# Performance work log

Hardware: AMD Instinct MI355X
Metric: run time of the kernel (lower is better)

The kernel has to match this reference:

```python
import jax, jax.numpy as jnp
import numpy as np

B = 8
C = 256
NS = [16384, 4096, 1024, 256, 1]  # point-pyramid sizes per level
D = 3                              # coordinate dim
EPS = (1e-06, 1e-06, 1e-06, 1e-06, 1e-06)


def _pm_level(x, coords_c, coords_n, idx, p_i, eps_i):
    """One hierarchical gather-weighted power-mean pooling step.
    x: (B, C, N)  coords_c: (B, N, D)  coords_n: (B, Nn, D)  idx: (B, N) in [0, Nn).
    Returns pooled features (B, C, Nn)."""
    Bq, Cq, N = x.shape
    Nn = coords_n.shape[1]
    Dd = coords_c.shape[-1]
    # gather parent coords for each child, delta to parent
    cn = jnp.take_along_axis(coords_n, idx[:, :, None], axis=1)            # (B,N,D)
    delta = coords_c - cn                                                   # (B,N,D)
    # per-parent max/min of delta (scatter_max / scatter_min)
    smax = jax.vmap(lambda d, ix: jax.ops.segment_max(d, ix, num_segments=Nn))(delta, idx)
    smin = jax.vmap(lambda d, ix: jax.ops.segment_min(d, ix, num_segments=Nn))(delta, idx)
    pos_ub = jnp.maximum(smax, 0.0)   # clamp(min=0)
    neg_lb = jnp.minimum(smin, 0.0)   # clamp(max=0)
    # gather bounds back to children, pick by sign of delta
    pos_g = jnp.take_along_axis(pos_ub, idx[:, :, None], axis=1)
    neg_g = jnp.take_along_axis(neg_lb, idx[:, :, None], axis=1)
    inuse = jnp.where(delta >= 0.0, pos_g, neg_g)
    w = 1.0 - jnp.abs(delta) / (jnp.abs(inuse) + 1e-6)                      # (B,N,D)
    # split channels across the D coordinate weights: [q, q, ..., q+r]
    q, r = Cq // Dd, Cq % Dd
    reps = np.asarray([q] * (Dd - 1) + [q + r])
    w_c = jnp.repeat(w, reps, axis=-1, total_repeat_length=Cq)              # (B,N,C)
    x_pow = jnp.maximum(x, eps_i) ** p_i                                    # (B,C,N)
    xw = x_pow.transpose(0, 2, 1) * w_c                                     # (B,N,C)
    # scatter_sum of weighted powers and of weights, per parent cell
    xw_s = jax.vmap(lambda a, ix: jax.ops.segment_sum(a, ix, num_segments=Nn))(xw, idx)   # (B,Nn,C)
    w_s = jax.vmap(lambda a, ix: jax.ops.segment_sum(a, ix, num_segments=Nn))(w_c, idx)   # (B,Nn,C)
    nxt = (xw_s / (w_s + 1e-6)) ** (1.0 / p_i)
    return nxt.transpose(0, 2, 1)                                           # (B,C,Nn)


def setup_inputs() -> dict:
    key = jax.random.key(0)
    ks = jax.random.split(key, 16)
    x = jax.random.normal(ks[0], (B, C, NS[0]), dtype=jnp.float32)
    coords = [jax.random.normal(ks[1 + i], (B, NS[i], D), dtype=jnp.float32) for i in range(5)]
    idxs = []
    for i in range(4):
        # every parent gets ~NS[i]/NS[i+1] children; permute per batch for irregular access
        base = jnp.arange(NS[i], dtype=jnp.int32) % NS[i + 1]
        bk = jax.random.split(ks[6 + i], B)
        idxs.append(jax.vmap(lambda k: jax.random.permutation(k, base))(bk))
    p = jnp.full((5,), 3.0, dtype=jnp.float32)
    return {"x": x,
            "idx0": idxs[0], "idx1": idxs[1], "idx2": idxs[2], "idx3": idxs[3],
            "coords0": coords[0], "coords1": coords[1], "coords2": coords[2],
            "coords3": coords[3], "coords4": coords[4],
            "p": p}


def reference(x, idx0, idx1, idx2, idx3, coords0, coords1, coords2, coords3, coords4, p):
    idxs = (idx0, idx1, idx2, idx3)
    coords = (coords0, coords1, coords2, coords3, coords4)
    cur = x
    for i in range(4):
        cur = _pm_level(cur, coords[i], coords[i + 1], idxs[i], p[i], EPS[i])
    return cur[..., 0]  # squeeze (B,C,1) -> (B,C)
```

## Files before the change

### kernel.cpp

```cpp
#include <hip/hip_runtime.h>
#include <math.h>

constexpr int B  = 8;
constexpr int C  = 256;
constexpr int Q  = 85;
constexpr int NS0 = 16384, NS1 = 4096, NS2 = 1024, NS3 = 256;
constexpr int PAR = NS1 + NS2 + NS3;
constexpr int SLT = NS0 + NS1 + NS2;

__device__ __forceinline__ int cdim(int c) {
    int d = c / Q;
    return d > 2 ? 2 : d;
}

__device__ __forceinline__ void sib_w(float4 c0, float4 c1, float4 c2, float4 c3,
                                      int target,
                                      float& wt0, float& wt1, float& wt2,
                                      float& zs0, float& zs1, float& zs2) {
    float mx0 = fmaxf(fmaxf(c0.x, c1.x), fmaxf(c2.x, c3.x));
    float mn0 = fminf(fminf(c0.x, c1.x), fminf(c2.x, c3.x));
    float mx1 = fmaxf(fmaxf(c0.y, c1.y), fmaxf(c2.y, c3.y));
    float mn1 = fminf(fminf(c0.y, c1.y), fminf(c2.y, c3.y));
    float mx2 = fmaxf(fmaxf(c0.z, c1.z), fmaxf(c2.z, c3.z));
    float mn2 = fminf(fminf(c0.z, c1.z), fminf(c2.z, c3.z));
    float pos0 = fmaxf(mx0, 0.f), neg0 = fminf(mn0, 0.f);
    float pos1 = fmaxf(mx1, 0.f), neg1 = fminf(mn1, 0.f);
    float pos2 = fmaxf(mx2, 0.f), neg2 = fminf(mn2, 0.f);

    zs0 = zs1 = zs2 = 0.f;
    wt0 = wt1 = wt2 = 0.f;
    float4 chs[4] = {c0, c1, c2, c3};
#pragma unroll
    for (int k = 0; k < 4; ++k) {
        float d0 = chs[k].x, d1 = chs[k].y, d2 = chs[k].z;
        int   n  = __float_as_int(chs[k].w);
        float wv0 = 1.f - fabsf(d0) / (fabsf(d0 >= 0.f ? pos0 : neg0) + 1e-6f);
        float wv1 = 1.f - fabsf(d1) / (fabsf(d1 >= 0.f ? pos1 : neg1) + 1e-6f);
        float wv2 = 1.f - fabsf(d2) / (fabsf(d2 >= 0.f ? pos2 : neg2) + 1e-6f);
        zs0 += wv0; zs1 += wv1; zs2 += wv2;
        if (n == target) { wt0 = wv0; wt1 = wv1; wt2 = wv2; }
    }
}

__global__ void invert_fused_kernel(const int* __restrict__ idx0,
                                    const int* __restrict__ idx1,
                                    const int* __restrict__ idx2,
                                    const float* __restrict__ c0,
                                    const float* __restrict__ c1,
                                    const float* __restrict__ c2,
                                    const float* __restrict__ c3,
                                    const float* __restrict__ c4,
                                    unsigned* __restrict__ cnt,
                                    float4*   __restrict__ dslot,
                                    float*    __restrict__ w3,
                                    float*    __restrict__ z4) {
    __shared__ float sm[3][256];
    __shared__ float sn[3][256];

    if (blockIdx.y == 3) {
        if (blockIdx.x >= 8) return;
        int b = blockIdx.x;
        int n = threadIdx.x;

        float pc0 = c4[b * 3 + 0], pc1 = c4[b * 3 + 1], pc2 = c4[b * 3 + 2];
        const float* cp = &c3[((size_t)(b * 256 + n)) * 3];
        float d0 = cp[0] - pc0, d1 = cp[1] - pc1, d2 = cp[2] - pc2;
        sm[0][n] = d0; sm[1][n] = d1; sm[2][n] = d2;
        sn[0][n] = d0; sn[1][n] = d1; sn[2][n] = d2;
        __syncthreads();
        for (int s = 128; s > 0; s >>= 1) {
            if (n < s) {
#pragma unroll
                for (int d = 0; d < 3; ++d) {
                    sm[d][n] = fmaxf(sm[d][n], sm[d][n + s]);
                    sn[d][n] = fminf(sn[d][n], sn[d][n + s]);
                }
            }
            __syncthreads();
        }
        float pos0 = fmaxf(sm[0][0], 0.f), pos1 = fmaxf(sm[1][0], 0.f), pos2 = fmaxf(sm[2][0], 0.f);
        float neg0 = fminf(sn[0][0], 0.f), neg1 = fminf(sn[1][0], 0.f), neg2 = fminf(sn[2][0], 0.f);
        __syncthreads();

        float w0 = 1.f - fabsf(d0) / (fabsf(d0 >= 0.f ? pos0 : neg0) + 1e-6f);
        float w1 = 1.f - fabsf(d1) / (fabsf(d1 >= 0.f ? pos1 : neg1) + 1e-6f);
        float w2 = 1.f - fabsf(d2) / (fabsf(d2 >= 0.f ? pos2 : neg2) + 1e-6f);
        float* wp = &w3[((size_t)(b * 256 + n)) * 3];
        wp[0] = w0; wp[1] = w1; wp[2] = w2;

        sm[0][n] = w0; sm[1][n] = w1; sm[2][n] = w2;
        __syncthreads();
        for (int s = 128; s > 0; s >>= 1) {
            if (n < s) {
#pragma unroll
                for (int d = 0; d < 3; ++d) sm[d][n] += sm[d][n + s];
            }
            __syncthreads();
        }
        if (n == 0) {
            z4[b * 3 + 0] = sm[0][0];
            z4[b * 3 + 1] = sm[1][0];
            z4[b * 3 + 2] = sm[2][0];
        }
        return;
    }

    int lvl = blockIdx.y;
    const int*   idx = (lvl == 0) ? idx0 : (lvl == 1 ? idx1 : idx2);
    const float* cc  = (lvl == 0) ? c0   : (lvl == 1 ? c1   : c2);
    const float* cn  = (lvl == 0) ? c1   : (lvl == 1 ? c2   : c3);
    int N  = (lvl == 0) ? NS0 : (lvl == 1 ? NS1 : NS2);
    int Nn = (lvl == 0) ? NS1 : (lvl == 1 ? NS2 : NS3);
    int cbase = (lvl == 0) ? 0 : (lvl == 1 ? NS1 : NS1 + NS2);
    int sbase = (lvl == 0) ? 0 : (lvl == 1 ? NS0 : NS0 + NS1);

    int t = blockIdx.x * blockDim.x + threadIdx.x;
    if (t >= B * N) return;
    int b = t / N;
    int n = t - b * N;
    int j = idx[t];
    int pj = b * Nn + j;

    unsigned o = atomicAdd(&cnt[(size_t)b * PAR + cbase + j], 1u);
    int slot = (int)(o & 3u);

    float4 dv;
    dv.x = cc[(size_t)t * 3 + 0] - cn[(size_t)pj * 3 + 0];
    dv.y = cc[(size_t)t * 3 + 1] - cn[(size_t)pj * 3 + 1];
    dv.z = cc[(size_t)t * 3 + 2] - cn[(size_t)pj * 3 + 2];
    dv.w = __int_as_float(n);
    dslot[((size_t)b * SLT + sbase + (size_t)j * 4) + slot] = dv;
}

__global__ void leafwn_kernel(const float4* __restrict__ dslot,
                              const int*   __restrict__ idx1,
                              const int*   __restrict__ idx2,
                              const float* __restrict__ w3,
                              const float* __restrict__ z4,
                              float* __restrict__ Wn) {
    int t = blockIdx.x * blockDim.x + threadIdx.x;
    if (t >= B * NS1) return;
    int b = t / NS1;
    int j = t - b * NS1;

    const float4* dp0 = &dslot[(size_t)b * SLT + (size_t)j * 4];
    float4 l0 = dp0[0], l1 = dp0[1], l2 = dp0[2], l3 = dp0[3];

    float mx0 = fmaxf(fmaxf(l0.x, l1.x), fmaxf(l2.x, l3.x));
    float mn0 = fminf(fminf(l0.x, l1.x), fminf(l2.x, l3.x));
    float mx1 = fmaxf(fmaxf(l0.y, l1.y), fmaxf(l2.y, l3.y));
    float mn1 = fminf(fminf(l0.y, l1.y), fminf(l2.y, l3.y));
    float mx2 = fmaxf(fmaxf(l0.z, l1.z), fmaxf(l2.z, l3.z));
    float mn2 = fminf(fminf(l0.z, l1.z), fminf(l2.z, l3.z));
    float pos0 = fmaxf(mx0, 0.f), neg0 = fminf(mn0, 0.f);
    float pos1 = fmaxf(mx1, 0.f), neg1 = fminf(mn1, 0.f);
    float pos2 = fmaxf(mx2, 0.f), neg2 = fminf(mn2, 0.f);

    float wv0[4], wv1[4], wv2[4];
    int   nid[4];
    float zz0 = 0.f, zz1 = 0.f, zz2 = 0.f;
    float4 chs[4] = {l0, l1, l2, l3};
#pragma unroll
    for (int k = 0; k < 4; ++k) {
        float d0 = chs[k].x, d1 = chs[k].y, d2 = chs[k].z;
        nid[k] = __float_as_int(chs[k].w);
        wv0[k] = 1.f - fabsf(d0) / (fabsf(d0 >= 0.f ? pos0 : neg0) + 1e-6f);
        wv1[k] = 1.f - fabsf(d1) / (fabsf(d1 >= 0.f ? pos1 : neg1) + 1e-6f);
        wv2[k] = 1.f - fabsf(d2) / (fabsf(d2 >= 0.f ? pos2 : neg2) + 1e-6f);
        zz0 += wv0[k]; zz1 += wv1[k]; zz2 += wv2[k];
    }

    int a2 = idx1[t];
    const float4* dp1 = &dslot[(size_t)b * SLT + NS0 + (size_t)a2 * 4];
    float w1t0, w1t1, w1t2, z20, z21, z22;
    sib_w(dp1[0], dp1[1], dp1[2], dp1[3], j, w1t0, w1t1, w1t2, z20, z21, z22);

    int a3 = idx2[(size_t)b * NS2 + a2];
    const float4* dp2 = &dslot[(size_t)b * SLT + NS0 + NS1 + (size_t)a3 * 4];
    float w2t0, w2t1, w2t2, z30, z31, z32;
    sib_w(dp2[0], dp2[1], dp2[2], dp2[3], a2, w2t0, w2t1, w2t2, z30, z31, z32);

    const float* w3p = &w3[((size_t)b * 256 + a3) * 3];
    float U0 = w1t0 / (z20 + 1e-6f) * w2t0 / (z30 + 1e-6f) * w3p[0] / (z4[b * 3 + 0] + 1e-6f);
    float U1 = w1t1 / (z21 + 1e-6f) * w2t1 / (z31 + 1e-6f) * w3p[1] / (z4[b * 3 + 1] + 1e-6f);
    float U2 = w1t2 / (z22 + 1e-6f) * w2t2 / (z32 + 1e-6f) * w3p[2] / (z4[b * 3 + 2] + 1e-6f);

    float r0 = U0 / (zz0 + 1e-6f);
    float r1 = U1 / (zz1 + 1e-6f);
    float r2 = U2 / (zz2 + 1e-6f);

    float* Wb0 = Wn + ((size_t)(b * 3 + 0)) * NS0;
    float* Wb1 = Wn + ((size_t)(b * 3 + 1)) * NS0;
    float* Wb2 = Wn + ((size_t)(b * 3 + 2)) * NS0;
#pragma unroll
    for (int k = 0; k < 4; ++k) {
        int n = nid[k];
        Wb0[n] = wv0[k] * r0;
        Wb1[n] = wv1[k] * r1;
        Wb2[n] = wv2[k] * r2;
    }
}

__global__ void final_kernel(const float* __restrict__ x,
                             const float* __restrict__ Wn,
                             float* __restrict__ out,
                             const float* __restrict__ p_arr) {
    __shared__ float sred[256];
    int bc = blockIdx.x;
    int b = bc / C;
    int c = bc - b * C;
    int d = cdim(c);
    float p = p_arr[0];
    bool p3 = (p == 3.0f);

    const float4* xr = (const float4*)(x + (size_t)bc * NS0);
    const float4* wr = (const float4*)(Wn + ((size_t)(b * 3 + d)) * NS0);

    float acc = 0.f;
#pragma unroll 8
    for (int i = threadIdx.x; i < NS0 / 4; i += 256) {
        float4 xv = xr[i];
        float4 wv = wr[i];
        float v0 = fmaxf(xv.x, 1e-6f);
        float v1 = fmaxf(xv.y, 1e-6f);
        float v2 = fmaxf(xv.z, 1e-6f);
        float v3 = fmaxf(xv.w, 1e-6f);
        float s0 = p3 ? v0 * v0 * v0 : powf(v0, p);
        float s1 = p3 ? v1 * v1 * v1 : powf(v1, p);
        float s2 = p3 ? v2 * v2 * v2 : powf(v2, p);
        float s3 = p3 ? v3 * v3 * v3 : powf(v3, p);
        acc = fmaf(s0, wv.x, acc);
        acc = fmaf(s1, wv.y, acc);
        acc = fmaf(s2, wv.z, acc);
        acc = fmaf(s3, wv.w, acc);
    }
    sred[threadIdx.x] = acc;
    __syncthreads();
    for (int s = 128; s > 0; s >>= 1) {
        if (threadIdx.x < s) sred[threadIdx.x] += sred[threadIdx.x + s];
        __syncthreads();
    }
    if (threadIdx.x == 0) {
        float t = sred[0];
        out[bc] = p3 ? cbrtf(t) : powf(t, 1.0f / p);
    }
}

extern "C" void kernel_launch(void* const* d_in, const int* in_sizes, int n_in,
                              void* d_out, int out_size, void* d_ws, size_t ws_size,
                              hipStream_t stream) {
    const float* x      = (const float*)d_in[0];
    const int*   idx0   = (const int*)d_in[1];
    const int*   idx1   = (const int*)d_in[2];
    const int*   idx2   = (const int*)d_in[3];
    const float* coords0 = (const float*)d_in[5];
    const float* coords1 = (const float*)d_in[6];
    const float* coords2 = (const float*)d_in[7];
    const float* coords3 = (const float*)d_in[8];
    const float* coords4 = (const float*)d_in[9];
    const float* p = (const float*)d_in[10];

    char* ws = (char*)d_ws;
    size_t off = 0;
    auto alloc = [&](size_t bytes) -> void* {
        off = (off + 255) & ~(size_t)255;
        void* r = ws + off;
        off += bytes;
        return r;
    };

    unsigned* cnt  = (unsigned*)alloc((size_t)B * PAR * sizeof(unsigned));
    float4*  dslot = (float4*)alloc((size_t)B * SLT * sizeof(float4));
    float* w3 = (float*)alloc((size_t)B * NS3 * 3 * sizeof(float));
    float* z4 = (float*)alloc((size_t)B * 1   * 3 * sizeof(float));
    float* Wn = (float*)alloc((size_t)B * 3 * NS0 * sizeof(float));

    dim3 ig((B * NS0 + 255) / 256, 4);
    invert_fused_kernel<<<ig, 256, 0, stream>>>(
        idx0, idx1, idx2, coords0, coords1, coords2, coords3, coords4,
        cnt, dslot, w3, z4);

    leafwn_kernel<<<(B * NS1 + 255) / 256, 256, 0, stream>>>(
        dslot, idx1, idx2, w3, z4, Wn);

    final_kernel<<<B * C, 256, 0, stream>>>(x, Wn, (float*)d_out, p);
}
```

Baseline: 48.98 us.

## Fuse leaf-weight computation and final reduction into one chunked mega kernel

Merges the leaf-weight kernel and the per-channel reduction kernel into one kernel. Each block recomputes the composite leaf weights for a 512-point chunk into shared memory, then reduces x over its channel range using wave shuffles and global atomics. A last-block counter applies the final cube root. This removes the Wn global buffer round trip and one launch. In exchange it adds atomics, per-block weight recomputation, and a reduction order that is no longer deterministic.

```diff
diff --git a/kernel.cpp b/kernel.cpp
--- a/kernel.cpp
+++ b/kernel.cpp
@@ -7,39 +7,31 @@
 constexpr int NS0 = 16384, NS1 = 4096, NS2 = 1024, NS3 = 256;
 constexpr int PAR = NS1 + NS2 + NS3;
 constexpr int SLT = NS0 + NS1 + NS2;
-
-__device__ __forceinline__ int cdim(int c) {
-    int d = c / Q;
-    return d > 2 ? 2 : d;
-}
-
-__device__ __forceinline__ void sib_w(float4 c0, float4 c1, float4 c2, float4 c3,
-                                      int target,
-                                      float& wt0, float& wt1, float& wt2,
-                                      float& zs0, float& zs1, float& zs2) {
-    float mx0 = fmaxf(fmaxf(c0.x, c1.x), fmaxf(c2.x, c3.x));
-    float mn0 = fminf(fminf(c0.x, c1.x), fminf(c2.x, c3.x));
-    float mx1 = fmaxf(fmaxf(c0.y, c1.y), fmaxf(c2.y, c3.y));
-    float mn1 = fminf(fminf(c0.y, c1.y), fminf(c2.y, c3.y));
-    float mx2 = fmaxf(fmaxf(c0.z, c1.z), fmaxf(c2.z, c3.z));
-    float mn2 = fminf(fminf(c0.z, c1.z), fminf(c2.z, c3.z));
-    float pos0 = fmaxf(mx0, 0.f), neg0 = fminf(mn0, 0.f);
-    float pos1 = fmaxf(mx1, 0.f), neg1 = fminf(mn1, 0.f);
-    float pos2 = fmaxf(mx2, 0.f), neg2 = fminf(mn2, 0.f);
-
-    zs0 = zs1 = zs2 = 0.f;
-    wt0 = wt1 = wt2 = 0.f;
-    float4 chs[4] = {c0, c1, c2, c3};
-#pragma unroll
-    for (int k = 0; k < 4; ++k) {
-        float d0 = chs[k].x, d1 = chs[k].y, d2 = chs[k].z;
-        int   n  = __float_as_int(chs[k].w);
-        float wv0 = 1.f - fabsf(d0) / (fabsf(d0 >= 0.f ? pos0 : neg0) + 1e-6f);
-        float wv1 = 1.f - fabsf(d1) / (fabsf(d1 >= 0.f ? pos1 : neg1) + 1e-6f);
-        float wv2 = 1.f - fabsf(d2) / (fabsf(d2 >= 0.f ? pos2 : neg2) + 1e-6f);
-        zs0 += wv0; zs1 += wv1; zs2 += wv2;
-        if (n == target) { wt0 = wv0; wt1 = wv1; wt2 = wv2; }
-    }
+constexpr int CH  = 512;
+constexpr int NCH = NS0 / CH;
+constexpr int MEGA_GRID = B * 3 * NCH;
+
+__device__ __forceinline__ void sib1(const float* __restrict__ base, int d,
+                                     int target, float& wt, float& zs) {
+    float v0 = base[0 * 4 + d], v1 = base[1 * 4 + d];
+    float v2 = base[2 * 4 + d], v3 = base[3 * 4 + d];
+    int i0 = __float_as_int(base[0 * 4 + 3]);
+    int i1 = __float_as_int(base[1 * 4 + 3]);
+    int i2 = __float_as_int(base[2 * 4 + 3]);
+    int i3 = __float_as_int(base[3 * 4 + 3]);
+    float mx = fmaxf(fmaxf(v0, v1), fmaxf(v2, v3));
+    float mn = fminf(fminf(v0, v1), fminf(v2, v3));
+    float pos = fmaxf(mx, 0.f), neg = fminf(mn, 0.f);
+    float w0 = 1.f - fabsf(v0) / (fabsf(v0 >= 0.f ? pos : neg) + 1e-6f);
+    float w1 = 1.f - fabsf(v1) / (fabsf(v1 >= 0.f ? pos : neg) + 1e-6f);
+    float w2 = 1.f - fabsf(v2) / (fabsf(v2 >= 0.f ? pos : neg) + 1e-6f);
+    float w3 = 1.f - fabsf(v3) / (fabsf(v3 >= 0.f ? pos : neg) + 1e-6f);
+    zs = w0 + w1 + w2 + w3;
+    wt = 0.f;
+    if (i0 == target) wt = w0;
+    if (i1 == target) wt = w1;
+    if (i2 == target) wt = w2;
+    if (i3 == target) wt = w3;
 }
 
 __global__ void invert_fused_kernel(const int* __restrict__ idx0,
@@ -53,11 +45,19 @@
                                     unsigned* __restrict__ cnt,
                                     float4*   __restrict__ dslot,
                                     float*    __restrict__ w3,
-                                    float*    __restrict__ z4) {
+                                    float*    __restrict__ z4,
+                                    float*    __restrict__ accum,
+                                    unsigned* __restrict__ counter) {
     __shared__ float sm[3][256];
     __shared__ float sn[3][256];
 
     if (blockIdx.y == 3) {
+        if (blockIdx.x == 8) {
+            int i = threadIdx.x;
+            for (; i < B * C; i += 256) accum[i] = 0.f;
+            if (threadIdx.x == 0) *counter = 0u;
+            return;
+        }
         if (blockIdx.x >= 8) return;
         int b = blockIdx.x;
         int n = threadIdx.x;
@@ -132,117 +132,92 @@
     dslot[((size_t)b * SLT + sbase + (size_t)j * 4) + slot] = dv;
 }
 
-__global__ void leafwn_kernel(const float4* __restrict__ dslot,
-                              const int*   __restrict__ idx1,
-                              const int*   __restrict__ idx2,
-                              const float* __restrict__ w3,
-                              const float* __restrict__ z4,
-                              float* __restrict__ Wn) {
-    int t = blockIdx.x * blockDim.x + threadIdx.x;
-    if (t >= B * NS1) return;
-    int b = t / NS1;
-    int j = t - b * NS1;
-
-    const float4* dp0 = &dslot[(size_t)b * SLT + (size_t)j * 4];
-    float4 l0 = dp0[0], l1 = dp0[1], l2 = dp0[2], l3 = dp0[3];
-
-    float mx0 = fmaxf(fmaxf(l0.x, l1.x), fmaxf(l2.x, l3.x));
-    float mn0 = fminf(fminf(l0.x, l1.x), fminf(l2.x, l3.x));
-    float mx1 = fmaxf(fmaxf(l0.y, l1.y), fmaxf(l2.y, l3.y));
-    float mn1 = fminf(fminf(l0.y, l1.y), fminf(l2.y, l3.y));
-    float mx2 = fmaxf(fmaxf(l0.z, l1.z), fmaxf(l2.z, l3.z));
-    float mn2 = fminf(fminf(l0.z, l1.z), fminf(l2.z, l3.z));
-    float pos0 = fmaxf(mx0, 0.f), neg0 = fminf(mn0, 0.f);
-    float pos1 = fmaxf(mx1, 0.f), neg1 = fminf(mn1, 0.f);
-    float pos2 = fmaxf(mx2, 0.f), neg2 = fminf(mn2, 0.f);
-
-    float wv0[4], wv1[4], wv2[4];
-    int   nid[4];
-    float zz0 = 0.f, zz1 = 0.f, zz2 = 0.f;
-    float4 chs[4] = {l0, l1, l2, l3};
-#pragma unroll
-    for (int k = 0; k < 4; ++k) {
-        float d0 = chs[k].x, d1 = chs[k].y, d2 = chs[k].z;
-        nid[k] = __float_as_int(chs[k].w);
-        wv0[k] = 1.f - fabsf(d0) / (fabsf(d0 >= 0.f ? pos0 : neg0) + 1e-6f);
-        wv1[k] = 1.f - fabsf(d1) / (fabsf(d1 >= 0.f ? pos1 : neg1) + 1e-6f);
-        wv2[k] = 1.f - fabsf(d2) / (fabsf(d2 >= 0.f ? pos2 : neg2) + 1e-6f);
-        zz0 += wv0[k]; zz1 += wv1[k]; zz2 += wv2[k];
-    }
-
-    int a2 = idx1[t];
-    const float4* dp1 = &dslot[(size_t)b * SLT + NS0 + (size_t)a2 * 4];
-    float w1t0, w1t1, w1t2, z20, z21, z22;
-    sib_w(dp1[0], dp1[1], dp1[2], dp1[3], j, w1t0, w1t1, w1t2, z20, z21, z22);
-
-    int a3 = idx2[(size_t)b * NS2 + a2];
-    const float4* dp2 = &dslot[(size_t)b * SLT + NS0 + NS1 + (size_t)a3 * 4];
-    float w2t0, w2t1, w2t2, z30, z31, z32;
-    sib_w(dp2[0], dp2[1], dp2[2], dp2[3], a2, w2t0, w2t1, w2t2, z30, z31, z32);
-
-    const float* w3p = &w3[((size_t)b * 256 + a3) * 3];
-    float U0 = w1t0 / (z20 + 1e-6f) * w2t0 / (z30 + 1e-6f) * w3p[0] / (z4[b * 3 + 0] + 1e-6f);
-    float U1 = w1t1 / (z21 + 1e-6f) * w2t1 / (z31 + 1e-6f) * w3p[1] / (z4[b * 3 + 1] + 1e-6f);
-    float U2 = w1t2 / (z22 + 1e-6f) * w2t2 / (z32 + 1e-6f) * w3p[2] / (z4[b * 3 + 2] + 1e-6f);
-
-    float r0 = U0 / (zz0 + 1e-6f);
-    float r1 = U1 / (zz1 + 1e-6f);
-    float r2 = U2 / (zz2 + 1e-6f);
-
-    float* Wb0 = Wn + ((size_t)(b * 3 + 0)) * NS0;
-    float* Wb1 = Wn + ((size_t)(b * 3 + 1)) * NS0;
-    float* Wb2 = Wn + ((size_t)(b * 3 + 2)) * NS0;
-#pragma unroll
-    for (int k = 0; k < 4; ++k) {
-        int n = nid[k];
-        Wb0[n] = wv0[k] * r0;
-        Wb1[n] = wv1[k] * r1;
-        Wb2[n] = wv2[k] * r2;
-    }
-}
-
-__global__ void final_kernel(const float* __restrict__ x,
-                             const float* __restrict__ Wn,
-                             float* __restrict__ out,
-                             const float* __restrict__ p_arr) {
-    __shared__ float sred[256];
-    int bc = blockIdx.x;
-    int b = bc / C;
-    int c = bc - b * C;
-    int d = cdim(c);
+__global__ __launch_bounds__(256)
+void mega_kernel(const float* __restrict__ x,
+                 const int*   __restrict__ idx0,
+                 const int*   __restrict__ idx1,
+                 const int*   __restrict__ idx2,
+                 const float4* __restrict__ dslot,
+                 const float* __restrict__ w3,
+                 const float* __restrict__ z4,
+                 float*    __restrict__ accum,
+                 unsigned* __restrict__ counter,
+                 float*    __restrict__ out,
+                 const float* __restrict__ p_arr) {
+    __shared__ float Wl[CH];
+    __shared__ int lastflag;
+    int bi = blockIdx.x;
+    int b = bi / (3 * NCH);
+    int r = bi - b * (3 * NCH);
+    int d = r / NCH;
+    int chunk = r - d * NCH;
+    int n0 = chunk * CH;
+    int tid = threadIdx.x;
+
     float p = p_arr[0];
     bool p3 = (p == 3.0f);
-
-    const float4* xr = (const float4*)(x + (size_t)bc * NS0);
-    const float4* wr = (const float4*)(Wn + ((size_t)(b * 3 + d)) * NS0);
-
-    float acc = 0.f;
-#pragma unroll 8
-    for (int i = threadIdx.x; i < NS0 / 4; i += 256) {
-        float4 xv = xr[i];
-        float4 wv = wr[i];
-        float v0 = fmaxf(xv.x, 1e-6f);
-        float v1 = fmaxf(xv.y, 1e-6f);
-        float v2 = fmaxf(xv.z, 1e-6f);
-        float v3 = fmaxf(xv.w, 1e-6f);
-        float s0 = p3 ? v0 * v0 * v0 : powf(v0, p);
-        float s1 = p3 ? v1 * v1 * v1 : powf(v1, p);
-        float s2 = p3 ? v2 * v2 * v2 : powf(v2, p);
-        float s3 = p3 ? v3 * v3 * v3 : powf(v3, p);
-        acc = fmaf(s0, wv.x, acc);
-        acc = fmaf(s1, wv.y, acc);
-        acc = fmaf(s2, wv.z, acc);
-        acc = fmaf(s3, wv.w, acc);
-    }
-    sred[threadIdx.x] = acc;
+    float z4v = z4[b * 3 + d];
+    const float* ds = (const float*)dslot;
+    const size_t dsb = (size_t)b * SLT * 4;
+
+#pragma unroll
+    for (int it = 0; it < CH / 256; ++it) {
+        int li = tid + it * 256;
+        int n = n0 + li;
+        int j = idx0[(size_t)b * NS0 + n];
+        float wt, zz;
+        sib1(ds + dsb + (size_t)j * 16, d, n, wt, zz);
+        int a2 = idx1[(size_t)b * NS1 + j];
+        float w1t, z2;
+        sib1(ds + dsb + (size_t)(NS0 + a2 * 4) * 4, d, j, w1t, z2);
+        int a3 = idx2[(size_t)b * NS2 + a2];
+        float w2t, z3;
+        sib1(ds + dsb + (size_t)(NS0 + NS1 + a3 * 4) * 4, d, a2, w2t, z3);
+        float w3v = w3[((size_t)b * 256 + a3) * 3 + d];
+        Wl[li] = wt / (zz + 1e-6f) * w1t / (z2 + 1e-6f)
+               * w2t / (z3 + 1e-6f) * w3v / (z4v + 1e-6f);
+    }
     __syncthreads();
-    for (int s = 128; s > 0; s >>= 1) {
-        if (threadIdx.x < s) sred[threadIdx.x] += sred[threadIdx.x + s];
-        __syncthreads();
-    }
-    if (threadIdx.x == 0) {
-        float t = sred[0];
-        out[bc] = p3 ? cbrtf(t) : powf(t, 1.0f / p);
+
+    int lane = tid & 63;
+    int cslot = tid >> 6;
+    float4 wa = ((const float4*)Wl)[lane];
+    float4 wb = ((const float4*)Wl)[lane + 64];
+    int c_lo = d * Q;
+    int c_hi = (d == 2) ? C : c_lo + Q;
+    for (int c = c_lo + cslot; c < c_hi; c += 4) {
+        const float4* xr = (const float4*)(x + ((size_t)(b * C + c)) * NS0 + n0);
+        float4 xa = xr[lane];
+        float4 xb = xr[lane + 64];
+        float a0 = fmaxf(xa.x, 1e-6f), a1 = fmaxf(xa.y, 1e-6f);
+        float a2v = fmaxf(xa.z, 1e-6f), a3v = fmaxf(xa.w, 1e-6f);
+        float b0 = fmaxf(xb.x, 1e-6f), b1 = fmaxf(xb.y, 1e-6f);
+        float b2 = fmaxf(xb.z, 1e-6f), b3 = fmaxf(xb.w, 1e-6f);
+        float s0, s1, s2, s3, t0, t1, t2, t3;
+        if (p3) {
+            s0 = a0*a0*a0; s1 = a1*a1*a1; s2 = a2v*a2v*a2v; s3 = a3v*a3v*a3v;
+            t0 = b0*b0*b0; t1 = b1*b1*b1; t2 = b2*b2*b2; t3 = b3*b3*b3;
+        } else {
+            s0 = powf(a0, p); s1 = powf(a1, p); s2 = powf(a2v, p); s3 = powf(a3v, p);
+            t0 = powf(b0, p); t1 = powf(b1, p); t2 = powf(b2, p); t3 = powf(b3, p);
+        }
+        float acc = s0 * wa.x + s1 * wa.y + s2 * wa.z + s3 * wa.w
+                  + t0 * wb.x + t1 * wb.y + t2 * wb.z + t3 * wb.w;
+        for (int o = 32; o > 0; o >>= 1) acc += __shfl_down(acc, o, 64);
+        if (lane == 0) atomicAdd(&accum[b * C + c], acc);
+    }
+
+    __threadfence();
+    if (tid == 0) {
+        unsigned old = atomicAdd(counter, 1u);
+        lastflag = (old == (unsigned)(gridDim.x - 1)) ? 1 : 0;
+    }
+    __syncthreads();
+    if (lastflag) {
+        for (int i = tid; i < B * C; i += 256) {
+            float v = atomicAdd(&accum[i], 0.0f);
+            out[i] = p3 ? cbrtf(v) : powf(v, 1.0f / p);
+        }
     }
 }
 
@@ -269,19 +244,18 @@
         return r;
     };
 
-    unsigned* cnt  = (unsigned*)alloc((size_t)B * PAR * sizeof(unsigned));
-    float4*  dslot = (float4*)alloc((size_t)B * SLT * sizeof(float4));
-    float* w3 = (float*)alloc((size_t)B * NS3 * 3 * sizeof(float));
-    float* z4 = (float*)alloc((size_t)B * 1   * 3 * sizeof(float));
-    float* Wn = (float*)alloc((size_t)B * 3 * NS0 * sizeof(float));
+    unsigned* cnt   = (unsigned*)alloc((size_t)B * PAR * sizeof(unsigned));
+    float4*   dslot = (float4*)alloc((size_t)B * SLT * sizeof(float4));
+    float* w3    = (float*)alloc((size_t)B * NS3 * 3 * sizeof(float));
+    float* z4    = (float*)alloc((size_t)B * 1   * 3 * sizeof(float));
+    float* accum = (float*)alloc((size_t)B * C * sizeof(float));
+    unsigned* counter = (unsigned*)alloc(256);
 
     dim3 ig((B * NS0 + 255) / 256, 4);
     invert_fused_kernel<<<ig, 256, 0, stream>>>(
         idx0, idx1, idx2, coords0, coords1, coords2, coords3, coords4,
-        cnt, dslot, w3, z4);
-
-    leafwn_kernel<<<(B * NS1 + 255) / 256, 256, 0, stream>>>(
-        dslot, idx1, idx2, w3, z4, Wn);
-
-    final_kernel<<<B * C, 256, 0, stream>>>(x, Wn, (float*)d_out, p);
-}
+        cnt, dslot, w3, z4, accum, counter);
+
+    mega_kernel<<<MEGA_GRID, 256, 0, stream>>>(
+        x, idx0, idx1, idx2, dslot, w3, z4, accum, counter, (float*)d_out, p);
+}
```

After: 146.7 us. +199.5%, slower.
